# Kernel tuning notes

Measured on AMD Instinct MI355X. Metric: run time of the kernel, lower is better.

Reference implementation:

```python
import jax, jax.numpy as jnp
import numpy as np

B, F, D, R, U = 65536, 8, 2, 10, 32  # batch, leaves, local_dim, rank, units


def setup_inputs() -> dict:
    key = jax.random.key(0)
    ks = jax.random.split(key, 9)
    s = 0.3  # glorot-ish scale for tiny tensors
    return {
        "X": jax.random.normal(ks[0], (B, F, D), dtype=jnp.float32),
        "core11": jax.random.normal(ks[1], (R, R, R), dtype=jnp.float32) * s,
        "core12": jax.random.normal(ks[2], (R, R, R), dtype=jnp.float32) * s,
        "core13": jax.random.normal(ks[3], (R, R, R), dtype=jnp.float32) * s,
        "core14": jax.random.normal(ks[4], (R, R, R), dtype=jnp.float32) * s,
        "core21": jax.random.normal(ks[5], (R, R, R), dtype=jnp.float32) * s,
        "core22": jax.random.normal(ks[6], (R, R, R), dtype=jnp.float32) * s,
        "factor_matrices": jax.random.normal(ks[7], (D, R, F, U), dtype=jnp.float32) * s,
        "matrix_top": jax.random.normal(ks[8], (R, R), dtype=jnp.float32) * s,
    }


def _pair(a, b, core):
    # con[j] = sum_{i,k} a[i] * b[k] * core[i,k,j]  (per unit u, batch b)
    return jnp.einsum('ubi,ubk,ikj->ubj', a, b, core)


def reference(X, core11, core12, core13, core14, core21, core22,
              factor_matrices, matrix_top):
    # leaf contraction over local_dim, all units at once: [F, U, B, R]
    c = jnp.einsum('bfd,drfu->fubr', X, factor_matrices)
    # level 1 of the tree (pairs of leaves)
    p1 = _pair(c[0], c[1], core11)
    p2 = _pair(c[2], c[3], core12)
    p3 = _pair(c[4], c[5], core13)
    p4 = _pair(c[6], c[7], core14)
    # level 2
    q1 = _pair(p1, p2, core21)
    q2 = _pair(p3, p4, core22)
    # top: (q1 @ matrix_top) . q2 -> scalar per (unit, batch); activation is linear
    out = jnp.einsum('ubi,ij,ubj->bu', q1, matrix_top, q2)
    return out  # [B, U]
```

## Files before the change

### kernel.cpp

```cpp
#include <hip/hip_runtime.h>


#define BB 65536
#define FF 8
#define DD 2
#define RR 10
#define UU 32
#define UPT 2
#define BPT 2


__global__ __launch_bounds__(256) void precompute_T_fast(
    const float* __restrict__ core11, const float* __restrict__ core12,
    const float* __restrict__ core13, const float* __restrict__ core14,
    const float* __restrict__ core21, const float* __restrict__ core22,
    const float* __restrict__ FM, const float* __restrict__ MT,
    float* __restrict__ T)
{
    const int u   = blockIdx.x;
    const int tid = threadIdx.x;

    __shared__ float sC[6][RR * RR * RR];
    __shared__ float sMT[RR * RR];
    __shared__ float sLeaf[FF][2][RR];
    __shared__ float sP[4][4][RR];
    __shared__ float sQ[2][16][RR];
    __shared__ float sR1[16][RR];

#pragma unroll
    for (int r = 0; r < 4; ++r) {
        const int o = tid + 256 * r;
        if (o < RR * RR * RR) {
            sC[0][o] = core11[o];
            sC[1][o] = core12[o];
            sC[2][o] = core13[o];
            sC[3][o] = core14[o];
            sC[4][o] = core21[o];
            sC[5][o] = core22[o];
        }
    }
    if (tid < RR * RR) sMT[tid] = MT[tid];

    if (tid < FF * 2 * RR) {
        const int f = tid / (2 * RR);
        const int rem = tid % (2 * RR);
        const int a = rem / RR;
        const int r = rem % RR;
        sLeaf[f][a][r] = FM[((a * RR + r) * FF + f) * UU + u];
    }
    __syncthreads();

    if (tid < 4 * 4 * RR) {
        const int P   = tid / (4 * RR);
        const int rem = tid % (4 * RR);
        const int s   = rem / RR;
        const int j   = rem % RR;
        const int fa = 2 * P, fb = 2 * P + 1;
        const int ai = s & 1, bi = s >> 1;
        const float* cp = sC[P];
        float a[RR], b[RR];
#pragma unroll
        for (int i = 0; i < RR; ++i) { a[i] = sLeaf[fa][ai][i]; b[i] = sLeaf[fb][bi][i]; }
        float acc0 = 0.0f, acc1 = 0.0f;
#pragma unroll
        for (int i = 0; i < RR; ++i) {
#pragma unroll
            for (int k = 0; k < RR; ++k) {
                const float w = a[i] * b[k];
                const float c = cp[(i * RR + k) * RR + j];
                if (i & 1) acc1 = fmaf(w, c, acc1);
                else       acc0 = fmaf(w, c, acc0);
            }
        }
        sP[P][s][j] = acc0 + acc1;
    }
    __syncthreads();

    for (int t = tid; t < 2 * 16 * RR; t += 256) {
        const int side  = t / (16 * RR);
        const int rem   = t % (16 * RR);
        const int combo = rem / RR;
        const int j     = rem % RR;
        const int pa = side * 2, pb = side * 2 + 1;
        const float* cp = sC[4 + side];
        float a[RR], b[RR];
#pragma unroll
        for (int i = 0; i < RR; ++i) {
            a[i] = sP[pa][combo & 3][i];
            b[i] = sP[pb][combo >> 2][i];
        }
        float acc0 = 0.0f, acc1 = 0.0f;
#pragma unroll
        for (int i = 0; i < RR; ++i) {
#pragma unroll
            for (int k = 0; k < RR; ++k) {
                const float w = a[i] * b[k];
                const float c = cp[(i * RR + k) * RR + j];
                if (i & 1) acc1 = fmaf(w, c, acc1);
                else       acc0 = fmaf(w, c, acc0);
            }
        }
        sQ[side][combo][j] = acc0 + acc1;
    }
    __syncthreads();

    if (tid < 16 * RR) {
        const int p = tid / RR;
        const int j = tid % RR;
        float acc = 0.0f;
#pragma unroll
        for (int i = 0; i < RR; ++i)
            acc = fmaf(sQ[0][p][i], sMT[i * RR + j], acc);
        sR1[p][j] = acc;
    }
    __syncthreads();

    {
        const int c = tid;
        const int p = c & 15, q = c >> 4;
        float acc = 0.0f;
#pragma unroll
        for (int j = 0; j < RR; ++j)
            acc = fmaf(sR1[p][j], sQ[1][q][j], acc);
        T[u * 256 + c] = acc;
    }
}


__global__ __launch_bounds__(256, 4) void tree_eval(
    const float* __restrict__ X,
    const float* __restrict__ T,
    float* __restrict__ out)
{
    const int b0 = blockIdx.x * blockDim.x + threadIdx.x;
    const int u0 = blockIdx.y * UPT;

    const float* __restrict__ Ta = T + (u0 + 0) * 256;
    const float* __restrict__ Tb = T + (u0 + 1) * 256;

    float w1[BPT][16], w2[BPT][16];
#pragma unroll
    for (int bt = 0; bt < BPT; ++bt) {
        const int b = b0 + bt * (BB / BPT);
        const float4* xp = reinterpret_cast<const float4*>(X + (size_t)b * (FF * DD));
        float4 v0 = xp[0];
        float4 v1 = xp[1];
        float t01[4], t23[4];
#pragma unroll
        for (int a1 = 0; a1 < 2; ++a1)
#pragma unroll
            for (int a0 = 0; a0 < 2; ++a0) {
                const float xa0 = (a0 == 0) ? v0.x : v0.y;
                const float xa1 = (a1 == 0) ? v0.z : v0.w;
                const float xb0 = (a0 == 0) ? v1.x : v1.y;
                const float xb1 = (a1 == 0) ? v1.z : v1.w;
                t01[a1 * 2 + a0] = xa0 * xa1;
                t23[a1 * 2 + a0] = xb0 * xb1;
            }
#pragma unroll
        for (int p = 0; p < 16; ++p)
            w1[bt][p] = t01[p & 3] * t23[p >> 2];

        float4 v2 = xp[2];
        float4 v3 = xp[3];
        float t45[4], t67[4];
#pragma unroll
        for (int a1 = 0; a1 < 2; ++a1)
#pragma unroll
            for (int a0 = 0; a0 < 2; ++a0) {
                const float xa0 = (a0 == 0) ? v2.x : v2.y;
                const float xa1 = (a1 == 0) ? v2.z : v2.w;
                const float xb0 = (a0 == 0) ? v3.x : v3.y;
                const float xb1 = (a1 == 0) ? v3.z : v3.w;
                t45[a1 * 2 + a0] = xa0 * xa1;
                t67[a1 * 2 + a0] = xb0 * xb1;
            }
#pragma unroll
        for (int p = 0; p < 16; ++p)
            w2[bt][p] = t45[p & 3] * t67[p >> 2];
    }

    float accA[BPT], accB[BPT];
#pragma unroll
    for (int bt = 0; bt < BPT; ++bt) { accA[bt] = 0.0f; accB[bt] = 0.0f; }

#pragma unroll
    for (int q = 0; q < 16; ++q) {
        float sA[BPT], sB[BPT];
#pragma unroll
        for (int bt = 0; bt < BPT; ++bt) { sA[bt] = 0.0f; sB[bt] = 0.0f; }
#pragma unroll
        for (int p = 0; p < 16; ++p) {
            const float ta = Ta[q * 16 + p];
            const float tb = Tb[q * 16 + p];
#pragma unroll
            for (int bt = 0; bt < BPT; ++bt) {
                sA[bt] = fmaf(ta, w1[bt][p], sA[bt]);
                sB[bt] = fmaf(tb, w1[bt][p], sB[bt]);
            }
        }
#pragma unroll
        for (int bt = 0; bt < BPT; ++bt) {
            accA[bt] = fmaf(w2[bt][q], sA[bt], accA[bt]);
            accB[bt] = fmaf(w2[bt][q], sB[bt], accB[bt]);
        }
    }

#pragma unroll
    for (int bt = 0; bt < BPT; ++bt) {
        const int b = b0 + bt * (BB / BPT);
        float2 o;
        o.x = accA[bt];
        o.y = accB[bt];
        *reinterpret_cast<float2*>(out + (size_t)b * UU + u0) = o;
    }
}

extern "C" void kernel_launch(void* const* d_in, const int* in_sizes, int n_in,
                              void* d_out, int out_size, void* d_ws, size_t ws_size,
                              hipStream_t stream) {
    const float* X      = (const float*)d_in[0];
    const float* core11 = (const float*)d_in[1];
    const float* core12 = (const float*)d_in[2];
    const float* core13 = (const float*)d_in[3];
    const float* core14 = (const float*)d_in[4];
    const float* core21 = (const float*)d_in[5];
    const float* core22 = (const float*)d_in[6];
    const float* FM     = (const float*)d_in[7];
    const float* MT     = (const float*)d_in[8];
    float* out          = (float*)d_out;
    float* T            = (float*)d_ws;

    precompute_T_fast<<<dim3(UU), dim3(256), 0, stream>>>(
        core11, core12, core13, core14, core21, core22, FM, MT, T);

    tree_eval<<<dim3(BB / (256 * BPT), UU / UPT), dim3(256), 0, stream>>>(X, T, out);
}
```

Baseline: 100.9 us.

## Evaluate tree contraction with bf16x3 split MFMA instead of scalar FMAs

```diff
diff --git a/kernel.cpp b/kernel.cpp
--- a/kernel.cpp
+++ b/kernel.cpp
@@ -6,8 +6,16 @@
 #define DD 2
 #define RR 10
 #define UU 32
-#define UPT 2
-#define BPT 2
+
+typedef __attribute__((ext_vector_type(8))) short short8;
+typedef __attribute__((ext_vector_type(4))) float f32x4;
+
+__device__ __forceinline__ unsigned short f2bf_trunc(float x) {
+    return (unsigned short)(__builtin_bit_cast(unsigned int, x) >> 16);
+}
+__device__ __forceinline__ float bf2f(unsigned short h) {
+    return __builtin_bit_cast(float, ((unsigned int)h) << 16);
+}
 
 
 __global__ __launch_bounds__(256) void precompute_T_fast(
@@ -15,7 +23,7 @@
     const float* __restrict__ core13, const float* __restrict__ core14,
     const float* __restrict__ core21, const float* __restrict__ core22,
     const float* __restrict__ FM, const float* __restrict__ MT,
-    float* __restrict__ T)
+    unsigned short* __restrict__ Thi, unsigned short* __restrict__ Tlo)
 {
     const int u   = blockIdx.x;
     const int tid = threadIdx.x;
@@ -122,97 +130,88 @@
 #pragma unroll
         for (int j = 0; j < RR; ++j)
             acc = fmaf(sR1[p][j], sQ[1][q][j], acc);
-        T[u * 256 + c] = acc;
-    }
-}
-
-
-__global__ __launch_bounds__(256, 4) void tree_eval(
+        const unsigned short h = f2bf_trunc(acc);
+        const unsigned short l = f2bf_trunc(acc - bf2f(h));
+        Thi[u * 256 + c] = h;
+        Tlo[u * 256 + c] = l;
+    }
+}
+
+
+#define NWAVE 2048
+
+__global__ __launch_bounds__(256, 4) void tree_eval_mfma(
     const float* __restrict__ X,
-    const float* __restrict__ T,
+    const unsigned short* __restrict__ Thi,
+    const unsigned short* __restrict__ Tlo,
     float* __restrict__ out)
 {
-    const int b0 = blockIdx.x * blockDim.x + threadIdx.x;
-    const int u0 = blockIdx.y * UPT;
-
-    const float* __restrict__ Ta = T + (u0 + 0) * 256;
-    const float* __restrict__ Tb = T + (u0 + 1) * 256;
-
-    float w1[BPT][16], w2[BPT][16];
-#pragma unroll
-    for (int bt = 0; bt < BPT; ++bt) {
-        const int b = b0 + bt * (BB / BPT);
-        const float4* xp = reinterpret_cast<const float4*>(X + (size_t)b * (FF * DD));
-        float4 v0 = xp[0];
-        float4 v1 = xp[1];
-        float t01[4], t23[4];
-#pragma unroll
-        for (int a1 = 0; a1 < 2; ++a1)
-#pragma unroll
-            for (int a0 = 0; a0 < 2; ++a0) {
-                const float xa0 = (a0 == 0) ? v0.x : v0.y;
-                const float xa1 = (a1 == 0) ? v0.z : v0.w;
-                const float xb0 = (a0 == 0) ? v1.x : v1.y;
-                const float xb1 = (a1 == 0) ? v1.z : v1.w;
-                t01[a1 * 2 + a0] = xa0 * xa1;
-                t23[a1 * 2 + a0] = xb0 * xb1;
+    const int lane  = threadIdx.x & 63;
+    const int wid   = threadIdx.x >> 6;
+    const int gw    = blockIdx.x * 4 + wid;
+    const int ubase = blockIdx.y * 16;
+
+    const int n  = lane & 15;
+    const int kb = lane >> 4;
+
+    const unsigned short* th = Thi + (ubase + n) * 256 + kb * 8;
+    const unsigned short* tl = Tlo + (ubase + n) * 256 + kb * 8;
+
+    const int qpar = kb >> 1;
+    const int kpar = kb & 1;
+
+#pragma unroll
+    for (int it = 0; it < 2; ++it) {
+        const int bbase = (it * NWAVE + gw) * 16;
+
+        const float* xp = X + (size_t)(bbase + n) * (FF * DD);
+        const float4 v0 = *reinterpret_cast<const float4*>(xp + 0);
+        const float4 v1 = *reinterpret_cast<const float4*>(xp + 4);
+        const float4 v2 = *reinterpret_cast<const float4*>(xp + 8);
+        const float4 v3 = *reinterpret_cast<const float4*>(xp + 12);
+
+        float t01[4], t23[4], t45[4], t67[4];
+        t01[0] = v0.x * v0.z; t01[1] = v0.y * v0.z; t01[2] = v0.x * v0.w; t01[3] = v0.y * v0.w;
+        t23[0] = v1.x * v1.z; t23[1] = v1.y * v1.z; t23[2] = v1.x * v1.w; t23[3] = v1.y * v1.w;
+        t45[0] = v2.x * v2.z; t45[1] = v2.y * v2.z; t45[2] = v2.x * v2.w; t45[3] = v2.y * v2.w;
+        t67[0] = v3.x * v3.z; t67[1] = v3.y * v3.z; t67[2] = v3.x * v3.w; t67[3] = v3.y * v3.w;
+
+        const float v23_0 = kpar ? t23[2] : t23[0];
+        const float v23_1 = kpar ? t23[3] : t23[1];
+        float w1own[8];
+#pragma unroll
+        for (int j = 0; j < 8; ++j)
+            w1own[j] = t01[j & 3] * ((j >> 2) ? v23_1 : v23_0);
+
+        const float u45_0 = qpar ? t45[1] : t45[0];
+        const float u45_1 = qpar ? t45[3] : t45[2];
+
+        f32x4 acc = {0.0f, 0.0f, 0.0f, 0.0f};
+
+#pragma unroll
+        for (int s = 0; s < 8; ++s) {
+            const float w2s = ((s & 1) ? u45_1 : u45_0) * t67[s >> 1];
+
+            short8 ah, al;
+#pragma unroll
+            for (int j = 0; j < 8; ++j) {
+                const float a = w1own[j] * w2s;
+                const unsigned short h = f2bf_trunc(a);
+                ah[j] = (short)h;
+                al[j] = (short)f2bf_trunc(a - bf2f(h));
             }
-#pragma unroll
-        for (int p = 0; p < 16; ++p)
-            w1[bt][p] = t01[p & 3] * t23[p >> 2];
-
-        float4 v2 = xp[2];
-        float4 v3 = xp[3];
-        float t45[4], t67[4];
-#pragma unroll
-        for (int a1 = 0; a1 < 2; ++a1)
-#pragma unroll
-            for (int a0 = 0; a0 < 2; ++a0) {
-                const float xa0 = (a0 == 0) ? v2.x : v2.y;
-                const float xa1 = (a1 == 0) ? v2.z : v2.w;
-                const float xb0 = (a0 == 0) ? v3.x : v3.y;
-                const float xb1 = (a1 == 0) ? v3.z : v3.w;
-                t45[a1 * 2 + a0] = xa0 * xa1;
-                t67[a1 * 2 + a0] = xb0 * xb1;
-            }
-#pragma unroll
-        for (int p = 0; p < 16; ++p)
-            w2[bt][p] = t45[p & 3] * t67[p >> 2];
-    }
-
-    float accA[BPT], accB[BPT];
-#pragma unroll
-    for (int bt = 0; bt < BPT; ++bt) { accA[bt] = 0.0f; accB[bt] = 0.0f; }
-
-#pragma unroll
-    for (int q = 0; q < 16; ++q) {
-        float sA[BPT], sB[BPT];
-#pragma unroll
-        for (int bt = 0; bt < BPT; ++bt) { sA[bt] = 0.0f; sB[bt] = 0.0f; }
-#pragma unroll
-        for (int p = 0; p < 16; ++p) {
-            const float ta = Ta[q * 16 + p];
-            const float tb = Tb[q * 16 + p];
-#pragma unroll
-            for (int bt = 0; bt < BPT; ++bt) {
-                sA[bt] = fmaf(ta, w1[bt][p], sA[bt]);
-                sB[bt] = fmaf(tb, w1[bt][p], sB[bt]);
-            }
-        }
-#pragma unroll
-        for (int bt = 0; bt < BPT; ++bt) {
-            accA[bt] = fmaf(w2[bt][q], sA[bt], accA[bt]);
-            accB[bt] = fmaf(w2[bt][q], sB[bt], accB[bt]);
-        }
-    }
-
-#pragma unroll
-    for (int bt = 0; bt < BPT; ++bt) {
-        const int b = b0 + bt * (BB / BPT);
-        float2 o;
-        o.x = accA[bt];
-        o.y = accB[bt];
-        *reinterpret_cast<float2*>(out + (size_t)b * UU + u0) = o;
+            const short8 bh = *reinterpret_cast<const short8*>(th + s * 32);
+            const short8 bl = *reinterpret_cast<const short8*>(tl + s * 32);
+
+            acc = __builtin_amdgcn_mfma_f32_16x16x32_bf16(ah, bh, acc, 0, 0, 0);
+            acc = __builtin_amdgcn_mfma_f32_16x16x32_bf16(al, bh, acc, 0, 0, 0);
+            acc = __builtin_amdgcn_mfma_f32_16x16x32_bf16(ah, bl, acc, 0, 0, 0);
+        }
+
+        float* op = out + (size_t)(bbase + kb * 4) * UU + ubase + n;
+#pragma unroll
+        for (int r = 0; r < 4; ++r)
+            op[(size_t)r * UU] = acc[r];
     }
 }
 
@@ -229,10 +228,12 @@
     const float* FM     = (const float*)d_in[7];
     const float* MT     = (const float*)d_in[8];
     float* out          = (float*)d_out;
-    float* T            = (float*)d_ws;
+
+    unsigned short* Thi = (unsigned short*)d_ws;
+    unsigned short* Tlo = Thi + UU * 256;
 
     precompute_T_fast<<<dim3(UU), dim3(256), 0, stream>>>(
-        core11, core12, core13, core14, core21, core22, FM, MT, T);
-
-    tree_eval<<<dim3(BB / (256 * BPT), UU / UPT), dim3(256), 0, stream>>>(X, T, out);
-}
+        core11, core12, core13, core14, core21, core22, FM, MT, Thi, Tlo);
+
+    tree_eval_mfma<<<dim3(512, 2), dim3(256), 0, stream>>>(X, Thi, Tlo, out);
+}
```

Result: faster. 93.55 us (-7.3%).
